# Performance work log

Hardware: AMD Instinct MI355X
Metric: run time of the kernel (lower is better)

Reference implementation:

```python
import jax, jax.numpy as jnp
import numpy as np
import math

EMBED_DIM = 64
NUM_HEADS = 4
HEAD_DIM = EMBED_DIM // NUM_HEADS
TGT = 64
SRC = 64
BSZ = 128


def setup_inputs() -> dict:
    key = jax.random.key(0)
    ks = jax.random.split(key, 8)
    x = jax.random.normal(ks[0], (TGT, BSZ, EMBED_DIM), dtype=jnp.float32)
    relation = jax.random.normal(ks[1], (TGT, SRC, BSZ, EMBED_DIM), dtype=jnp.float32)
    in_proj_weight = jax.random.normal(ks[2], (3 * EMBED_DIM, EMBED_DIM), dtype=jnp.float32) * 0.02
    in_proj_bias = jnp.zeros((3 * EMBED_DIM,), dtype=jnp.float32)
    rel_weight = jax.random.normal(ks[3], (2 * EMBED_DIM, EMBED_DIM), dtype=jnp.float32) * 0.02
    rel_bias = jnp.zeros((2 * EMBED_DIM,), dtype=jnp.float32)
    out_weight = jax.random.normal(ks[4], (EMBED_DIM, EMBED_DIM), dtype=jnp.float32) * 0.02
    out_bias = jnp.zeros((EMBED_DIM,), dtype=jnp.float32)
    return {
        'query': x, 'key': x, 'value': x, 'relation': relation,
        'in_proj_weight': in_proj_weight, 'in_proj_bias': in_proj_bias,
        'rel_weight': rel_weight, 'rel_bias': rel_bias,
        'out_weight': out_weight, 'out_bias': out_bias,
    }


def reference(query, key, value, relation, in_proj_weight, in_proj_bias,
              rel_weight, rel_bias, out_weight, out_bias):
    E, H, hd = EMBED_DIM, NUM_HEADS, HEAD_DIM
    t, b, _ = query.shape
    s = key.shape[0]
    scaling = hd ** (-0.5)
    # qkv projections (slices of the fused in_proj weight, as in _in_proj)
    q = query @ in_proj_weight[:E].T + in_proj_bias[:E]
    k = key @ in_proj_weight[E:2 * E].T + in_proj_bias[E:2 * E]
    v = value @ in_proj_weight[2 * E:].T + in_proj_bias[2 * E:]
    q = q.reshape(t, b * H, hd)
    k = k.reshape(s, b * H, hd)
    v = v.reshape(s, b * H, hd)
    # relation projection -> ra, rb, each [t, s, b*H, hd], then transpose(0,1)
    rel = relation @ rel_weight.T + rel_bias  # [t, s, b, 2E]
    ra = rel[..., :E].reshape(t, s, b * H, hd).swapaxes(0, 1)  # [s, t, bH, hd]
    rb = rel[..., E:].reshape(t, s, b * H, hd).swapaxes(0, 1)
    # q[i,j] = q[i] + ra_t[i,j]; requires t == s (broadcast as in torch)
    qp = (q[:, None] + ra) * scaling            # [t, s, bH, hd]
    kp = k[None, :] + rb                        # [t, s, bH, hd]
    attn_weights = jnp.einsum('ijbn,ijbn->ijb', qp, kp) * (1.0 / math.sqrt(hd))
    attn_weights = jax.nn.softmax(attn_weights, axis=1)
    attn = jnp.einsum('ijb,jbn->bin', attn_weights, v)  # [bH, t, hd]
    attn = attn.swapaxes(0, 1).reshape(t, b, E)
    out = attn @ out_weight.T + out_bias
    return out
```

## Files before the change

### kernel.cpp

```cpp
#include <hip/hip_runtime.h>
#include <hip/hip_bf16.h>

#define T_ 64
#define S_ 64
#define B_ 128
#define E_ 64
#define H_ 4

typedef float f32x4 __attribute__((ext_vector_type(4)));
typedef short bf16x8 __attribute__((ext_vector_type(8)));

static __device__ __forceinline__ short f2b(float f) {
    union { __hip_bfloat16 h; short s; } u;
    u.h = __float2bfloat16(f);
    return u.s;
}

__global__ __launch_bounds__(256) void k_qkv(
    const float* __restrict__ qin, const float* __restrict__ kin,
    const float* __restrict__ vin, const float* __restrict__ W,
    const float* __restrict__ bias, float* __restrict__ qkv)
{
    __shared__ float xs[3][32 * 68];
    __shared__ float WTs[64 * 68];
    const int tid = threadIdx.x;
    const int row0 = blockIdx.x * 32;

    #pragma unroll
    for (int l = 0; l < 6; ++l) {
        int f4 = l * 256 + tid;
        int src = f4 >> 9, rem = f4 & 511;
        int r = rem >> 4, e0 = (rem & 15) << 2;
        const float* xin = (src == 0) ? qin : (src == 1 ? kin : vin);
        float4 xv = reinterpret_cast<const float4*>(xin)[(size_t)(row0 + r) * 16 + (e0 >> 2)];
        float* dst = &xs[src][r * 68];
        dst[e0] = xv.x; dst[e0 + 1] = xv.y; dst[e0 + 2] = xv.z; dst[e0 + 3] = xv.w;
    }

    const int rq = tid >> 5, og = tid & 31;
    const int r0 = rq * 4, op0 = og * 2;

    for (int seg = 0; seg < 3; ++seg) {
        __syncthreads();
        #pragma unroll
        for (int l = 0; l < 4; ++l) {
            int f4 = l * 256 + tid;
            int o = f4 >> 4, e0 = (f4 & 15) << 2;
            float4 wv = reinterpret_cast<const float4*>(W)[(size_t)(seg * 64 + o) * 16 + (e0 >> 2)];
            WTs[(e0 + 0) * 68 + o] = wv.x; WTs[(e0 + 1) * 68 + o] = wv.y;
            WTs[(e0 + 2) * 68 + o] = wv.z; WTs[(e0 + 3) * 68 + o] = wv.w;
        }
        __syncthreads();

        float acc[4][2];
        #pragma unroll
        for (int rr = 0; rr < 4; ++rr) {
            acc[rr][0] = bias[seg * 64 + op0];
            acc[rr][1] = bias[seg * 64 + op0 + 1];
        }
        const float* xsrc = xs[seg];
        #pragma unroll 4
        for (int e = 0; e < 64; ++e) {
            float w0 = WTs[e * 68 + op0];
            float w1 = WTs[e * 68 + op0 + 1];
            #pragma unroll
            for (int rr = 0; rr < 4; ++rr) {
                float xv = xsrc[(r0 + rr) * 68 + e];
                acc[rr][0] += xv * w0;
                acc[rr][1] += xv * w1;
            }
        }
        #pragma unroll
        for (int rr = 0; rr < 4; ++rr) {
            float2 ov = make_float2(acc[rr][0], acc[rr][1]);
            reinterpret_cast<float2*>(
                &qkv[((size_t)seg * T_ * B_ + row0 + r0 + rr) * E_ + op0])[0] = ov;
        }
    }
}

__global__ __launch_bounds__(512, 2) void k_logits_mfma(
    const float* __restrict__ rel, const float* __restrict__ relW,
    const float* __restrict__ relBias, const float* __restrict__ qkv,
    float* __restrict__ logits)
{
    __shared__ char Bs[16384];

    const int tid = threadIdx.x;
    const int w   = tid >> 6;
    const int l   = tid & 63;
    const int c   = l & 15;
    const int rq  = l >> 4;
    const int i   = blockIdx.x >> 3;
    const int jb  = (blockIdx.x & 7) * 8;

    #pragma unroll
    for (int li = 0; li < 4; ++li) {
        int f4 = li * 512 + tid;
        int o = f4 >> 4, e4 = f4 & 15;
        float4 wv = reinterpret_cast<const float4*>(relW)[f4];
        ushort4 bv;
        bv.x = (ushort)f2b(wv.x); bv.y = (ushort)f2b(wv.y);
        bv.z = (ushort)f2b(wv.z); bv.w = (ushort)f2b(wv.w);
        int ot = o >> 4, cc = o & 15;
        int ks = e4 >> 3, rqb = (e4 & 7) >> 1, half = e4 & 1;
        int dest = (ot * 2 + ks) * 1024 + (rqb * 16 + cc) * 16 + half * 8;
        *reinterpret_cast<ushort4*>(Bs + dest) = bv;
    }

    float qpre[4][4], bbv[4];
    {
        const float* qrow = qkv + (size_t)i * (B_ * E_);
        #pragma unroll
        for (int h = 0; h < 4; ++h) {
            float ba = relBias[h * 16 + c];
            bbv[h] = relBias[64 + h * 16 + c];
            #pragma unroll
            for (int r = 0; r < 4; ++r) {
                int b = w * 16 + rq * 4 + r;
                qpre[h][r] = qrow[b * E_ + h * 16 + c] + ba;
            }
        }
    }
    __syncthreads();

    const int arow = ((w * 16 + c) * E_) + rq * 8;
    const int kbase = (w * 16 + rq * 4) * E_;

    float lbuf[8];
    float4 a0, a1, a2, a3;
    {
        const float* ab = rel + ((size_t)jb * S_ + i) * (size_t)(B_ * E_) + arow;
        a0 = *(const float4*)(ab);
        a1 = *(const float4*)(ab + 4);
        a2 = *(const float4*)(ab + 32);
        a3 = *(const float4*)(ab + 36);
    }

    #pragma unroll 1
    for (int t = 0; t < 8; ++t) {
        const int j = jb + t;

        bf16x8 af[2];
        {
            bf16x8 a;
            a[0] = f2b(a0.x); a[1] = f2b(a0.y); a[2] = f2b(a0.z); a[3] = f2b(a0.w);
            a[4] = f2b(a1.x); a[5] = f2b(a1.y); a[6] = f2b(a1.z); a[7] = f2b(a1.w);
            af[0] = a;
            a[0] = f2b(a2.x); a[1] = f2b(a2.y); a[2] = f2b(a2.z); a[3] = f2b(a2.w);
            a[4] = f2b(a3.x); a[5] = f2b(a3.y); a[6] = f2b(a3.z); a[7] = f2b(a3.w);
            af[1] = a;
        }

        if (t < 7) {
            const float* ab = rel + ((size_t)(j + 1) * S_ + i) * (size_t)(B_ * E_) + arow;
            a0 = *(const float4*)(ab);
            a1 = *(const float4*)(ab + 4);
            a2 = *(const float4*)(ab + 32);
            a3 = *(const float4*)(ab + 36);
        }

        float kvv[4][4];
        {
            const float* krow = qkv + ((size_t)(T_ * B_) + (size_t)j * B_) * E_ + kbase;
            #pragma unroll
            for (int h = 0; h < 4; ++h)
                #pragma unroll
                for (int r = 0; r < 4; ++r)
                    kvv[h][r] = krow[r * E_ + h * 16 + c];
        }

        f32x4 acc[8];
        #pragma unroll
        for (int ot = 0; ot < 8; ++ot) acc[ot] = (f32x4){0.f, 0.f, 0.f, 0.f};
        #pragma unroll
        for (int ot = 0; ot < 8; ++ot) {
            #pragma unroll
            for (int ks = 0; ks < 2; ++ks) {
                bf16x8 bfr = *(const bf16x8*)(Bs + (ot * 2 + ks) * 1024 + l * 16);
                acc[ot] = __builtin_amdgcn_mfma_f32_16x16x32_bf16(af[ks], bfr, acc[ot], 0, 0, 0);
            }
        }

        float v[16];
        #pragma unroll
        for (int h = 0; h < 4; ++h)
            #pragma unroll
            for (int r = 0; r < 4; ++r)
                v[h * 4 + r] = (qpre[h][r] + acc[h][r]) *
                               (kvv[h][r] + bbv[h] + acc[4 + h][r]);
        #pragma unroll
        for (int k = 0; k < 8; ++k) {
            float x = (c & 1) ? v[2 * k + 1] : v[2 * k];
            float y = (c & 1) ? v[2 * k] : v[2 * k + 1];
            v[k] = x + __shfl_xor(y, 1);
        }
        #pragma unroll
        for (int k = 0; k < 4; ++k) {
            float x = (c & 2) ? v[2 * k + 1] : v[2 * k];
            float y = (c & 2) ? v[2 * k] : v[2 * k + 1];
            v[k] = x + __shfl_xor(y, 2);
        }
        #pragma unroll
        for (int k = 0; k < 2; ++k) {
            float x = (c & 4) ? v[2 * k + 1] : v[2 * k];
            float y = (c & 4) ? v[2 * k] : v[2 * k + 1];
            v[k] = x + __shfl_xor(y, 4);
        }
        {
            float x = (c & 8) ? v[1] : v[0];
            float y = (c & 8) ? v[0] : v[1];
            lbuf[t] = (x + __shfl_xor(y, 8)) * 0.0625f;
        }
    }

    {
        const int hh = c >> 2, rr = c & 3;
        const int b = w * 16 + rq * 4 + rr;
        float* dst = &logits[(((size_t)i * B_ + b) * H_ + hh) * S_ + jb];
        *reinterpret_cast<float4*>(dst) = make_float4(lbuf[0], lbuf[1], lbuf[2], lbuf[3]);
        *reinterpret_cast<float4*>(dst + 4) = make_float4(lbuf[4], lbuf[5], lbuf[6], lbuf[7]);
    }
}

__global__ __launch_bounds__(256) void k_attn(
    const float* __restrict__ logits, const float* __restrict__ qkv,
    const float* __restrict__ Wout, const float* __restrict__ bout,
    float* __restrict__ out)
{
    __shared__ float wsm[4][H_][S_];
    __shared__ float ap[4][68];
    const int tid = threadIdx.x;
    const int i = blockIdx.x >> 5;
    const int bq = blockIdx.x & 31;
    const int w = tid >> 6, l = tid & 63;
    const int b = bq * 4 + w;

    const float* lg = logits + ((size_t)i * B_ + b) * H_ * S_;
    const int h = l >> 4, sub = l & 15;
    float v0 = lg[h * S_ + sub];
    float v1 = lg[h * S_ + sub + 16];
    float v2 = lg[h * S_ + sub + 32];
    float v3 = lg[h * S_ + sub + 48];
    float m = fmaxf(fmaxf(v0, v1), fmaxf(v2, v3));
    #pragma unroll
    for (int d = 1; d < 16; d <<= 1) m = fmaxf(m, __shfl_xor(m, d));
    float e0 = expf(v0 - m), e1 = expf(v1 - m), e2 = expf(v2 - m), e3 = expf(v3 - m);
    float ss = e0 + e1 + e2 + e3;
    #pragma unroll
    for (int d = 1; d < 16; d <<= 1) ss += __shfl_xor(ss, d);
    float inv = 1.0f / ss;
    wsm[w][h][sub] = e0 * inv;
    wsm[w][h][sub + 16] = e1 * inv;
    wsm[w][h][sub + 32] = e2 * inv;
    wsm[w][h][sub + 48] = e3 * inv;
    __syncthreads();

    const float* vbase = qkv + (size_t)2 * T_ * B_ * E_ + (size_t)b * E_;
    const float* wrow = &wsm[w][l >> 4][0];
    float acc = 0.f;
    #pragma unroll 4
    for (int j = 0; j < S_; ++j) acc += wrow[j] * vbase[(size_t)j * B_ * E_ + l];
    ap[w][l] = acc;
    __syncthreads();

    const float* wo = Wout + l * E_;
    const float* apw = ap[w];
    float oacc = bout[l];
    #pragma unroll 4
    for (int e = 0; e < E_; ++e) oacc += apw[e] * wo[e];
    out[((size_t)i * B_ + b) * E_ + l] = oacc;
}

extern "C" void kernel_launch(void* const* d_in, const int* in_sizes, int n_in,
                              void* d_out, int out_size, void* d_ws, size_t ws_size,
                              hipStream_t stream)
{
    const float* qin = (const float*)d_in[0];
    const float* kin = (const float*)d_in[1];
    const float* vin = (const float*)d_in[2];
    const float* rel = (const float*)d_in[3];
    const float* ipw = (const float*)d_in[4];
    const float* ipb = (const float*)d_in[5];
    const float* rw  = (const float*)d_in[6];
    const float* rb  = (const float*)d_in[7];
    const float* ow  = (const float*)d_in[8];
    const float* obias = (const float*)d_in[9];

    float* qkv = (float*)d_ws;
    float* logits = qkv + 3 * T_ * B_ * E_;
    float* out = (float*)d_out;

    k_qkv<<<dim3(256), dim3(256), 0, stream>>>(qin, kin, vin, ipw, ipb, qkv);
    k_logits_mfma<<<dim3(512), dim3(512), 0, stream>>>(rel, rw, rb, qkv, logits);
    k_attn<<<dim3(2048), dim3(256), 0, stream>>>(logits, qkv, ow, obias, out);
}
```

Measured before the change: 68.99 us.

## Double-buffer relation loads, hoist B fragments to registers in logits kernel

The logits kernel now prefetches relation rows two steps ahead using two register buffers and a manually 2x-unrolled loop. It hoists all B-operand weight fragments from LDS into registers once, instead of rereading them every iteration. Per-step logits go to an LDS scratch array rather than a register array. Launch bounds drop from two blocks per CU to one to make room for the extra registers, which lowers occupancy and latency hiding in exchange for deeper prefetch.

```diff
diff --git a/kernel.cpp b/kernel.cpp
--- a/kernel.cpp
+++ b/kernel.cpp
@@ -79,12 +79,13 @@
     }
 }
 
-__global__ __launch_bounds__(512, 2) void k_logits_mfma(
+__global__ __launch_bounds__(512, 1) void k_logits_mfma(
     const float* __restrict__ rel, const float* __restrict__ relW,
     const float* __restrict__ relBias, const float* __restrict__ qkv,
     float* __restrict__ logits)
 {
-    __shared__ char Bs[16384];
+    __shared__ char  Bs[16384];
+    __shared__ float llds[8][64][9];
 
     const int tid = threadIdx.x;
     const int w   = tid >> 6;
@@ -124,102 +125,109 @@
     }
     __syncthreads();
 
+    bf16x8 bfr[8][2];
+    #pragma unroll
+    for (int ot = 0; ot < 8; ++ot)
+        #pragma unroll
+        for (int ks = 0; ks < 2; ++ks)
+            bfr[ot][ks] = *(const bf16x8*)(Bs + (ot * 2 + ks) * 1024 + l * 16);
+
     const int arow = ((w * 16 + c) * E_) + rq * 8;
     const int kbase = (w * 16 + rq * 4) * E_;
 
-    float lbuf[8];
-    float4 a0, a1, a2, a3;
+#define LOADA(jj, X0, X1, X2, X3)                                              \
+    {                                                                          \
+        const float* ab = rel + ((size_t)(jj) * S_ + i) * (size_t)(B_ * E_) + arow; \
+        X0 = *(const float4*)(ab);                                             \
+        X1 = *(const float4*)(ab + 4);                                         \
+        X2 = *(const float4*)(ab + 32);                                        \
+        X3 = *(const float4*)(ab + 36);                                        \
+    }
+
+#define BODY(t, X0, X1, X2, X3)                                                \
+    {                                                                          \
+        const int j = jb + (t);                                                \
+        float kvv[4][4];                                                       \
+        {                                                                      \
+            const float* krow = qkv + ((size_t)(T_ * B_) + (size_t)j * B_) * E_ + kbase; \
+            _Pragma("unroll")                                                  \
+            for (int h = 0; h < 4; ++h)                                        \
+                _Pragma("unroll")                                              \
+                for (int r = 0; r < 4; ++r)                                    \
+                    kvv[h][r] = krow[r * E_ + h * 16 + c];                     \
+        }                                                                      \
+        bf16x8 af0, af1;                                                       \
+        {                                                                      \
+            bf16x8 a;                                                          \
+            a[0] = f2b(X0.x); a[1] = f2b(X0.y); a[2] = f2b(X0.z); a[3] = f2b(X0.w); \
+            a[4] = f2b(X1.x); a[5] = f2b(X1.y); a[6] = f2b(X1.z); a[7] = f2b(X1.w); \
+            af0 = a;                                                           \
+            a[0] = f2b(X2.x); a[1] = f2b(X2.y); a[2] = f2b(X2.z); a[3] = f2b(X2.w); \
+            a[4] = f2b(X3.x); a[5] = f2b(X3.y); a[6] = f2b(X3.z); a[7] = f2b(X3.w); \
+            af1 = a;                                                           \
+        }                                                                      \
+        if ((t) + 2 < 8) { LOADA(jb + (t) + 2, X0, X1, X2, X3) }               \
+        f32x4 acc[8];                                                          \
+        _Pragma("unroll")                                                      \
+        for (int ot = 0; ot < 8; ++ot) acc[ot] = (f32x4){0.f, 0.f, 0.f, 0.f};  \
+        _Pragma("unroll")                                                      \
+        for (int ot = 0; ot < 8; ++ot) {                                       \
+            acc[ot] = __builtin_amdgcn_mfma_f32_16x16x32_bf16(af0, bfr[ot][0], acc[ot], 0, 0, 0); \
+            acc[ot] = __builtin_amdgcn_mfma_f32_16x16x32_bf16(af1, bfr[ot][1], acc[ot], 0, 0, 0); \
+        }                                                                      \
+        float v[16];                                                           \
+        _Pragma("unroll")                                                      \
+        for (int h = 0; h < 4; ++h)                                            \
+            _Pragma("unroll")                                                  \
+            for (int r = 0; r < 4; ++r)                                        \
+                v[h * 4 + r] = (qpre[h][r] + acc[h][r]) *                      \
+                               (kvv[h][r] + bbv[h] + acc[4 + h][r]);           \
+        _Pragma("unroll")                                                      \
+        for (int k = 0; k < 8; ++k) {                                          \
+            float x = (c & 1) ? v[2 * k + 1] : v[2 * k];                       \
+            float y = (c & 1) ? v[2 * k] : v[2 * k + 1];                       \
+            v[k] = x + __shfl_xor(y, 1);                                       \
+        }                                                                      \
+        _Pragma("unroll")                                                      \
+        for (int k = 0; k < 4; ++k) {                                          \
+            float x = (c & 2) ? v[2 * k + 1] : v[2 * k];                       \
+            float y = (c & 2) ? v[2 * k] : v[2 * k + 1];                       \
+            v[k] = x + __shfl_xor(y, 2);                                       \
+        }                                                                      \
+        _Pragma("unroll")                                                      \
+        for (int k = 0; k < 2; ++k) {                                          \
+            float x = (c & 4) ? v[2 * k + 1] : v[2 * k];                       \
+            float y = (c & 4) ? v[2 * k] : v[2 * k + 1];                       \
+            v[k] = x + __shfl_xor(y, 4);                                       \
+        }                                                                      \
+        {                                                                      \
+            float x = (c & 8) ? v[1] : v[0];                                   \
+            float y = (c & 8) ? v[0] : v[1];                                   \
+            llds[w][l][(t)] = (x + __shfl_xor(y, 8)) * 0.0625f;                \
+        }                                                                      \
+    }
+
+    float4 aA0, aA1, aA2, aA3, aB0, aB1, aB2, aB3;
+    LOADA(jb + 0, aA0, aA1, aA2, aA3)
+    LOADA(jb + 1, aB0, aB1, aB2, aB3)
+
+    #pragma unroll 1
+    for (int tt = 0; tt < 8; tt += 2) {
+        BODY(tt,     aA0, aA1, aA2, aA3)
+        BODY(tt + 1, aB0, aB1, aB2, aB3)
+    }
+#undef BODY
+#undef LOADA
+
     {
-        const float* ab = rel + ((size_t)jb * S_ + i) * (size_t)(B_ * E_) + arow;
-        a0 = *(const float4*)(ab);
-        a1 = *(const float4*)(ab + 4);
-        a2 = *(const float4*)(ab + 32);
-        a3 = *(const float4*)(ab + 36);
-    }
-
-    #pragma unroll 1
-    for (int t = 0; t < 8; ++t) {
-        const int j = jb + t;
-
-        bf16x8 af[2];
-        {
-            bf16x8 a;
-            a[0] = f2b(a0.x); a[1] = f2b(a0.y); a[2] = f2b(a0.z); a[3] = f2b(a0.w);
-            a[4] = f2b(a1.x); a[5] = f2b(a1.y); a[6] = f2b(a1.z); a[7] = f2b(a1.w);
-            af[0] = a;
-            a[0] = f2b(a2.x); a[1] = f2b(a2.y); a[2] = f2b(a2.z); a[3] = f2b(a2.w);
-            a[4] = f2b(a3.x); a[5] = f2b(a3.y); a[6] = f2b(a3.z); a[7] = f2b(a3.w);
-            af[1] = a;
-        }
-
-        if (t < 7) {
-            const float* ab = rel + ((size_t)(j + 1) * S_ + i) * (size_t)(B_ * E_) + arow;
-            a0 = *(const float4*)(ab);
-            a1 = *(const float4*)(ab + 4);
-            a2 = *(const float4*)(ab + 32);
-            a3 = *(const float4*)(ab + 36);
-        }
-
-        float kvv[4][4];
-        {
-            const float* krow = qkv + ((size_t)(T_ * B_) + (size_t)j * B_) * E_ + kbase;
-            #pragma unroll
-            for (int h = 0; h < 4; ++h)
-                #pragma unroll
-                for (int r = 0; r < 4; ++r)
-                    kvv[h][r] = krow[r * E_ + h * 16 + c];
-        }
-
-        f32x4 acc[8];
-        #pragma unroll
-        for (int ot = 0; ot < 8; ++ot) acc[ot] = (f32x4){0.f, 0.f, 0.f, 0.f};
-        #pragma unroll
-        for (int ot = 0; ot < 8; ++ot) {
-            #pragma unroll
-            for (int ks = 0; ks < 2; ++ks) {
-                bf16x8 bfr = *(const bf16x8*)(Bs + (ot * 2 + ks) * 1024 + l * 16);
-                acc[ot] = __builtin_amdgcn_mfma_f32_16x16x32_bf16(af[ks], bfr, acc[ot], 0, 0, 0);
-            }
-        }
-
-        float v[16];
-        #pragma unroll
-        for (int h = 0; h < 4; ++h)
-            #pragma unroll
-            for (int r = 0; r < 4; ++r)
-                v[h * 4 + r] = (qpre[h][r] + acc[h][r]) *
-                               (kvv[h][r] + bbv[h] + acc[4 + h][r]);
-        #pragma unroll
-        for (int k = 0; k < 8; ++k) {
-            float x = (c & 1) ? v[2 * k + 1] : v[2 * k];
-            float y = (c & 1) ? v[2 * k] : v[2 * k + 1];
-            v[k] = x + __shfl_xor(y, 1);
-        }
-        #pragma unroll
-        for (int k = 0; k < 4; ++k) {
-            float x = (c & 2) ? v[2 * k + 1] : v[2 * k];
-            float y = (c & 2) ? v[2 * k] : v[2 * k + 1];
-            v[k] = x + __shfl_xor(y, 2);
-        }
-        #pragma unroll
-        for (int k = 0; k < 2; ++k) {
-            float x = (c & 4) ? v[2 * k + 1] : v[2 * k];
-            float y = (c & 4) ? v[2 * k] : v[2 * k + 1];
-            v[k] = x + __shfl_xor(y, 4);
-        }
-        {
-            float x = (c & 8) ? v[1] : v[0];
-            float y = (c & 8) ? v[0] : v[1];
-            lbuf[t] = (x + __shfl_xor(y, 8)) * 0.0625f;
-        }
-    }
-
-    {
+        float f[8];
+        #pragma unroll
+        for (int t2 = 0; t2 < 8; ++t2) f[t2] = llds[w][l][t2];
         const int hh = c >> 2, rr = c & 3;
         const int b = w * 16 + rq * 4 + rr;
         float* dst = &logits[(((size_t)i * B_ + b) * H_ + hh) * S_ + jb];
-        *reinterpret_cast<float4*>(dst) = make_float4(lbuf[0], lbuf[1], lbuf[2], lbuf[3]);
-        *reinterpret_cast<float4*>(dst + 4) = make_float4(lbuf[4], lbuf[5], lbuf[6], lbuf[7]);
+        *reinterpret_cast<float4*>(dst) = make_float4(f[0], f[1], f[2], f[3]);
+        *reinterpret_cast<float4*>(dst + 4) = make_float4(f[4], f[5], f[6], f[7]);
     }
 }
 
```

Result: no change. 70.24 us (+1.8%).

## Split logits kernel into one block per (i,j,half-batch) and relayout logits

Applied to the files above, without the earlier changes.

The logits kernel no longer loops over 8 source positions per block with software prefetch. Each 256-thread block now handles a single (i, j) pair and half the batch, launched as 8192 blocks. The logits buffer is laid out as [t][s][b*H] so each block writes one contiguous row, and the softmax kernel reads with a strided pattern to match. This buys more parallelism and latency hiding across blocks, at the cost of converting the rel weights to bf16 into shared memory once per block instead of once per 8 positions, and of uncoalesced logit reads in the attention kernel.

```diff
diff --git a/kernel.cpp b/kernel.cpp
--- a/kernel.cpp
+++ b/kernel.cpp
@@ -79,7 +79,7 @@
     }
 }
 
-__global__ __launch_bounds__(512, 2) void k_logits_mfma(
+__global__ __launch_bounds__(256, 3) void k_logits_mfma(
     const float* __restrict__ rel, const float* __restrict__ relW,
     const float* __restrict__ relBias, const float* __restrict__ qkv,
     float* __restrict__ logits)
@@ -91,12 +91,24 @@
     const int l   = tid & 63;
     const int c   = l & 15;
     const int rq  = l >> 4;
-    const int i   = blockIdx.x >> 3;
-    const int jb  = (blockIdx.x & 7) * 8;
-
-    #pragma unroll
-    for (int li = 0; li < 4; ++li) {
-        int f4 = li * 512 + tid;
+    const int g   = blockIdx.x & 1;
+    const int j   = (blockIdx.x >> 1) & 63;
+    const int i   = blockIdx.x >> 7;
+    const int btile = g * 4 + w;
+
+    const int arow = ((btile * 16 + c) * E_) + rq * 8;
+    float4 a0, a1, a2, a3;
+    {
+        const float* ab = rel + ((size_t)j * S_ + i) * (size_t)(B_ * E_) + arow;
+        a0 = *(const float4*)(ab);
+        a1 = *(const float4*)(ab + 4);
+        a2 = *(const float4*)(ab + 32);
+        a3 = *(const float4*)(ab + 36);
+    }
+
+    #pragma unroll
+    for (int li = 0; li < 8; ++li) {
+        int f4 = li * 256 + tid;
         int o = f4 >> 4, e4 = f4 & 15;
         float4 wv = reinterpret_cast<const float4*>(relW)[f4];
         ushort4 bv;
@@ -117,109 +129,80 @@
             bbv[h] = relBias[64 + h * 16 + c];
             #pragma unroll
             for (int r = 0; r < 4; ++r) {
-                int b = w * 16 + rq * 4 + r;
+                int b = btile * 16 + rq * 4 + r;
                 qpre[h][r] = qrow[b * E_ + h * 16 + c] + ba;
             }
         }
     }
     __syncthreads();
 
-    const int arow = ((w * 16 + c) * E_) + rq * 8;
-    const int kbase = (w * 16 + rq * 4) * E_;
-
-    float lbuf[8];
-    float4 a0, a1, a2, a3;
-    {
-        const float* ab = rel + ((size_t)jb * S_ + i) * (size_t)(B_ * E_) + arow;
-        a0 = *(const float4*)(ab);
-        a1 = *(const float4*)(ab + 4);
-        a2 = *(const float4*)(ab + 32);
-        a3 = *(const float4*)(ab + 36);
-    }
-
-    #pragma unroll 1
-    for (int t = 0; t < 8; ++t) {
-        const int j = jb + t;
-
-        bf16x8 af[2];
-        {
-            bf16x8 a;
-            a[0] = f2b(a0.x); a[1] = f2b(a0.y); a[2] = f2b(a0.z); a[3] = f2b(a0.w);
-            a[4] = f2b(a1.x); a[5] = f2b(a1.y); a[6] = f2b(a1.z); a[7] = f2b(a1.w);
-            af[0] = a;
-            a[0] = f2b(a2.x); a[1] = f2b(a2.y); a[2] = f2b(a2.z); a[3] = f2b(a2.w);
-            a[4] = f2b(a3.x); a[5] = f2b(a3.y); a[6] = f2b(a3.z); a[7] = f2b(a3.w);
-            af[1] = a;
-        }
-
-        if (t < 7) {
-            const float* ab = rel + ((size_t)(j + 1) * S_ + i) * (size_t)(B_ * E_) + arow;
-            a0 = *(const float4*)(ab);
-            a1 = *(const float4*)(ab + 4);
-            a2 = *(const float4*)(ab + 32);
-            a3 = *(const float4*)(ab + 36);
-        }
-
-        float kvv[4][4];
-        {
-            const float* krow = qkv + ((size_t)(T_ * B_) + (size_t)j * B_) * E_ + kbase;
-            #pragma unroll
-            for (int h = 0; h < 4; ++h)
-                #pragma unroll
-                for (int r = 0; r < 4; ++r)
-                    kvv[h][r] = krow[r * E_ + h * 16 + c];
-        }
-
-        f32x4 acc[8];
-        #pragma unroll
-        for (int ot = 0; ot < 8; ++ot) acc[ot] = (f32x4){0.f, 0.f, 0.f, 0.f};
-        #pragma unroll
-        for (int ot = 0; ot < 8; ++ot) {
-            #pragma unroll
-            for (int ks = 0; ks < 2; ++ks) {
-                bf16x8 bfr = *(const bf16x8*)(Bs + (ot * 2 + ks) * 1024 + l * 16);
-                acc[ot] = __builtin_amdgcn_mfma_f32_16x16x32_bf16(af[ks], bfr, acc[ot], 0, 0, 0);
-            }
-        }
-
-        float v[16];
+    float kvv[4][4];
+    {
+        const float* krow = qkv + ((size_t)(T_ * B_) + (size_t)j * B_ + btile * 16 + rq * 4) * E_;
         #pragma unroll
         for (int h = 0; h < 4; ++h)
             #pragma unroll
             for (int r = 0; r < 4; ++r)
-                v[h * 4 + r] = (qpre[h][r] + acc[h][r]) *
-                               (kvv[h][r] + bbv[h] + acc[4 + h][r]);
-        #pragma unroll
-        for (int k = 0; k < 8; ++k) {
-            float x = (c & 1) ? v[2 * k + 1] : v[2 * k];
-            float y = (c & 1) ? v[2 * k] : v[2 * k + 1];
-            v[k] = x + __shfl_xor(y, 1);
-        }
-        #pragma unroll
-        for (int k = 0; k < 4; ++k) {
-            float x = (c & 2) ? v[2 * k + 1] : v[2 * k];
-            float y = (c & 2) ? v[2 * k] : v[2 * k + 1];
-            v[k] = x + __shfl_xor(y, 2);
-        }
-        #pragma unroll
-        for (int k = 0; k < 2; ++k) {
-            float x = (c & 4) ? v[2 * k + 1] : v[2 * k];
-            float y = (c & 4) ? v[2 * k] : v[2 * k + 1];
-            v[k] = x + __shfl_xor(y, 4);
-        }
-        {
-            float x = (c & 8) ? v[1] : v[0];
-            float y = (c & 8) ? v[0] : v[1];
-            lbuf[t] = (x + __shfl_xor(y, 8)) * 0.0625f;
-        }
-    }
-
-    {
-        const int hh = c >> 2, rr = c & 3;
-        const int b = w * 16 + rq * 4 + rr;
-        float* dst = &logits[(((size_t)i * B_ + b) * H_ + hh) * S_ + jb];
-        *reinterpret_cast<float4*>(dst) = make_float4(lbuf[0], lbuf[1], lbuf[2], lbuf[3]);
-        *reinterpret_cast<float4*>(dst + 4) = make_float4(lbuf[4], lbuf[5], lbuf[6], lbuf[7]);
+                kvv[h][r] = krow[r * E_ + h * 16 + c];
+    }
+
+    bf16x8 af0, af1;
+    {
+        bf16x8 a;
+        a[0] = f2b(a0.x); a[1] = f2b(a0.y); a[2] = f2b(a0.z); a[3] = f2b(a0.w);
+        a[4] = f2b(a1.x); a[5] = f2b(a1.y); a[6] = f2b(a1.z); a[7] = f2b(a1.w);
+        af0 = a;
+        a[0] = f2b(a2.x); a[1] = f2b(a2.y); a[2] = f2b(a2.z); a[3] = f2b(a2.w);
+        a[4] = f2b(a3.x); a[5] = f2b(a3.y); a[6] = f2b(a3.z); a[7] = f2b(a3.w);
+        af1 = a;
+    }
+
+    f32x4 acc[8];
+    #pragma unroll
+    for (int ot = 0; ot < 8; ++ot) acc[ot] = (f32x4){0.f, 0.f, 0.f, 0.f};
+    #pragma unroll
+    for (int ot = 0; ot < 8; ++ot) {
+        bf16x8 b0 = *(const bf16x8*)(Bs + (ot * 2 + 0) * 1024 + l * 16);
+        bf16x8 b1 = *(const bf16x8*)(Bs + (ot * 2 + 1) * 1024 + l * 16);
+        acc[ot] = __builtin_amdgcn_mfma_f32_16x16x32_bf16(af0, b0, acc[ot], 0, 0, 0);
+        acc[ot] = __builtin_amdgcn_mfma_f32_16x16x32_bf16(af1, b1, acc[ot], 0, 0, 0);
+    }
+
+    float v[16];
+    #pragma unroll
+    for (int h = 0; h < 4; ++h)
+        #pragma unroll
+        for (int r = 0; r < 4; ++r)
+            v[h * 4 + r] = (qpre[h][r] + acc[h][r]) *
+                           (kvv[h][r] + bbv[h] + acc[4 + h][r]);
+    #pragma unroll
+    for (int k = 0; k < 8; ++k) {
+        float x = (c & 1) ? v[2 * k + 1] : v[2 * k];
+        float y = (c & 1) ? v[2 * k] : v[2 * k + 1];
+        v[k] = x + __shfl_xor(y, 1);
+    }
+    #pragma unroll
+    for (int k = 0; k < 4; ++k) {
+        float x = (c & 2) ? v[2 * k + 1] : v[2 * k];
+        float y = (c & 2) ? v[2 * k] : v[2 * k + 1];
+        v[k] = x + __shfl_xor(y, 2);
+    }
+    #pragma unroll
+    for (int k = 0; k < 2; ++k) {
+        float x = (c & 4) ? v[2 * k + 1] : v[2 * k];
+        float y = (c & 4) ? v[2 * k] : v[2 * k + 1];
+        v[k] = x + __shfl_xor(y, 4);
+    }
+    float outv;
+    {
+        float x = (c & 8) ? v[1] : v[0];
+        float y = (c & 8) ? v[0] : v[1];
+        outv = (x + __shfl_xor(y, 8)) * 0.0625f;
+    }
+
+    {
+        const int off = btile * 64 + rq * 16 + (c & 3) * 4 + (c >> 2);
+        logits[((size_t)i * S_ + j) * (B_ * H_) + off] = outv;
     }
 }
 
@@ -236,12 +219,12 @@
     const int w = tid >> 6, l = tid & 63;
     const int b = bq * 4 + w;
 
-    const float* lg = logits + ((size_t)i * B_ + b) * H_ * S_;
     const int h = l >> 4, sub = l & 15;
-    float v0 = lg[h * S_ + sub];
-    float v1 = lg[h * S_ + sub + 16];
-    float v2 = lg[h * S_ + sub + 32];
-    float v3 = lg[h * S_ + sub + 48];
+    const float* lg = logits + (size_t)i * S_ * (B_ * H_) + b * H_ + h;
+    float v0 = lg[(size_t)(sub +  0) * (B_ * H_)];
+    float v1 = lg[(size_t)(sub + 16) * (B_ * H_)];
+    float v2 = lg[(size_t)(sub + 32) * (B_ * H_)];
+    float v3 = lg[(size_t)(sub + 48) * (B_ * H_)];
     float m = fmaxf(fmaxf(v0, v1), fmaxf(v2, v3));
     #pragma unroll
     for (int d = 1; d < 16; d <<= 1) m = fmaxf(m, __shfl_xor(m, d));
@@ -292,6 +275,6 @@
     float* out = (float*)d_out;
 
     k_qkv<<<dim3(256), dim3(256), 0, stream>>>(qin, kin, vin, ipw, ipb, qkv);
-    k_logits_mfma<<<dim3(512), dim3(512), 0, stream>>>(rel, rw, rb, qkv, logits);
+    k_logits_mfma<<<dim3(8192), dim3(256), 0, stream>>>(rel, rw, rb, qkv, logits);
     k_attn<<<dim3(2048), dim3(256), 0, stream>>>(logits, qkv, ow, obias, out);
 }
```

Measured after the change: 78.36 us. +13.6%, slower.

## Precompute bf16 rel weights and fold key+bias into MFMA via identity matrix

Applied to the files above, without the earlier changes.

An extra block in the QKV kernel converts the relation weight to bf16 in MFMA fragment layout once and builds an identity block. The K projection plus relation bias is written as packed bf16 fragments. The logits kernel then copies the weights straight into LDS and adds k+bias with an extra MFMA against the identity matrix, instead of scattered fp32 K loads and per-block weight conversion. Logit results are staged through LDS instead of registers. This lowers register pressure and global gather traffic, at the cost of extra MFMAs and bf16 rounding of k+bias.

```diff
diff --git a/kernel.cpp b/kernel.cpp
--- a/kernel.cpp
+++ b/kernel.cpp
@@ -19,11 +19,39 @@
 __global__ __launch_bounds__(256) void k_qkv(
     const float* __restrict__ qin, const float* __restrict__ kin,
     const float* __restrict__ vin, const float* __restrict__ W,
-    const float* __restrict__ bias, float* __restrict__ qkv)
+    const float* __restrict__ bias, float* __restrict__ qkv,
+    const float* __restrict__ relW, const float* __restrict__ relBias,
+    ushort* __restrict__ wBf, unsigned int* __restrict__ kpbW)
 {
+    const int tid = threadIdx.x;
+
+    if (blockIdx.x == 256) {
+        #pragma unroll
+        for (int li = 0; li < 8; ++li) {
+            int f4 = li * 256 + tid;
+            int o = f4 >> 4, e4 = f4 & 15;
+            float4 wv = reinterpret_cast<const float4*>(relW)[f4];
+            ushort4 bv;
+            bv.x = (ushort)f2b(wv.x); bv.y = (ushort)f2b(wv.y);
+            bv.z = (ushort)f2b(wv.z); bv.w = (ushort)f2b(wv.w);
+            int ot = o >> 4, cc = o & 15;
+            int ks = e4 >> 3, rqb = (e4 & 7) >> 1, half = e4 & 1;
+            int dest = (ot * 2 + ks) * 512 + (rqb * 16 + cc) * 8 + half * 4;
+            *reinterpret_cast<ushort4*>(wBf + dest) = bv;
+        }
+        #pragma unroll
+        for (int li = 0; li < 8; ++li) {
+            int t = li * 256 + tid;
+            int ot = t >> 9, lane = (t >> 3) & 63, e = t & 7;
+            int cI = lane & 15, rqI = lane >> 4;
+            wBf[8192 + t] =
+                (rqI * 8 + e == (ot & 1) * 16 + cI) ? (ushort)0x3F80 : (ushort)0;
+        }
+        return;
+    }
+
     __shared__ float xs[3][32 * 68];
     __shared__ float WTs[64 * 68];
-    const int tid = threadIdx.x;
     const int row0 = blockIdx.x * 32;
 
     #pragma unroll
@@ -76,110 +104,119 @@
             reinterpret_cast<float2*>(
                 &qkv[((size_t)seg * T_ * B_ + row0 + r0 + rr) * E_ + op0])[0] = ov;
         }
+        if (seg == 1) {
+            #pragma unroll
+            for (int rr = 0; rr < 4; ++rr) {
+                int row = row0 + r0 + rr;
+                int jj = row >> 7, b = row & 127;
+                float kb0 = acc[rr][0] + relBias[64 + op0];
+                float kb1 = acc[rr][1] + relBias[64 + op0 + 1];
+                unsigned int u = (unsigned int)(ushort)f2b(kb0) |
+                                 ((unsigned int)(ushort)f2b(kb1) << 16);
+                int off = jj * 8192 + (op0 >> 5) * 4096 + (b >> 4) * 512 +
+                          ((b & 15) + ((op0 & 31) >> 3) * 16) * 8 + (op0 & 7);
+                kpbW[off >> 1] = u;
+            }
+        }
     }
 }
 
 __global__ __launch_bounds__(512, 2) void k_logits_mfma(
-    const float* __restrict__ rel, const float* __restrict__ relW,
-    const float* __restrict__ relBias, const float* __restrict__ qkv,
-    float* __restrict__ logits)
+    const float* __restrict__ rel, const ushort* __restrict__ wBf,
+    const ushort* __restrict__ kpbF, const float* __restrict__ relBias,
+    const float* __restrict__ qkv, float* __restrict__ logits)
 {
-    __shared__ char Bs[16384];
+    __shared__ char  Bs[20480];
+    __shared__ float llds[8][64][9];
 
     const int tid = threadIdx.x;
-    const int w   = tid >> 6;
-    const int l   = tid & 63;
-    const int c   = l & 15;
-    const int rq  = l >> 4;
-    const int i   = blockIdx.x >> 3;
-    const int jb  = (blockIdx.x & 7) * 8;
+    const int w = tid >> 6, l = tid & 63;
+    const int c = l & 15, rq = l >> 4;
+    const int i = blockIdx.x >> 3;
+    const int jb = (blockIdx.x & 7) * 8;
 
     #pragma unroll
-    for (int li = 0; li < 4; ++li) {
-        int f4 = li * 512 + tid;
-        int o = f4 >> 4, e4 = f4 & 15;
-        float4 wv = reinterpret_cast<const float4*>(relW)[f4];
-        ushort4 bv;
-        bv.x = (ushort)f2b(wv.x); bv.y = (ushort)f2b(wv.y);
-        bv.z = (ushort)f2b(wv.z); bv.w = (ushort)f2b(wv.w);
-        int ot = o >> 4, cc = o & 15;
-        int ks = e4 >> 3, rqb = (e4 & 7) >> 1, half = e4 & 1;
-        int dest = (ot * 2 + ks) * 1024 + (rqb * 16 + cc) * 16 + half * 8;
-        *reinterpret_cast<ushort4*>(Bs + dest) = bv;
-    }
-
-    float qpre[4][4], bbv[4];
+    for (int li = 0; li < 3; ++li) {
+        int idx = li * 512 + tid;
+        if (idx < 1280)
+            reinterpret_cast<float4*>(Bs)[idx] =
+                reinterpret_cast<const float4*>(wBf)[idx];
+    }
+
+    float qpre[4][4];
     {
         const float* qrow = qkv + (size_t)i * (B_ * E_);
         #pragma unroll
         for (int h = 0; h < 4; ++h) {
             float ba = relBias[h * 16 + c];
-            bbv[h] = relBias[64 + h * 16 + c];
             #pragma unroll
-            for (int r = 0; r < 4; ++r) {
-                int b = w * 16 + rq * 4 + r;
-                qpre[h][r] = qrow[b * E_ + h * 16 + c] + ba;
-            }
+            for (int r = 0; r < 4; ++r)
+                qpre[h][r] = qrow[(w * 16 + rq * 4 + r) * E_ + h * 16 + c] + ba;
         }
     }
     __syncthreads();
 
-    const int arow = ((w * 16 + c) * E_) + rq * 8;
-    const int kbase = (w * 16 + rq * 4) * E_;
-
-    float lbuf[8];
-    float4 a0, a1, a2, a3;
+    const int arow = (w * 16 + c) * E_ + rq * 8;
+    const int kfo  = w * 512 + l * 8;
+
+    float4 x0, x1, x2, x3;
     {
         const float* ab = rel + ((size_t)jb * S_ + i) * (size_t)(B_ * E_) + arow;
-        a0 = *(const float4*)(ab);
-        a1 = *(const float4*)(ab + 4);
-        a2 = *(const float4*)(ab + 32);
-        a3 = *(const float4*)(ab + 36);
+        x0 = *(const float4*)(ab);
+        x1 = *(const float4*)(ab + 4);
+        x2 = *(const float4*)(ab + 32);
+        x3 = *(const float4*)(ab + 36);
     }
 
     #pragma unroll 1
     for (int t = 0; t < 8; ++t) {
         const int j = jb + t;
 
-        bf16x8 af[2];
+        bf16x8 kf0 = *(const bf16x8*)(kpbF + (size_t)j * 8192 + kfo);
+        bf16x8 kf1 = *(const bf16x8*)(kpbF + (size_t)j * 8192 + 4096 + kfo);
+
+        bf16x8 af0, af1;
         {
             bf16x8 a;
-            a[0] = f2b(a0.x); a[1] = f2b(a0.y); a[2] = f2b(a0.z); a[3] = f2b(a0.w);
-            a[4] = f2b(a1.x); a[5] = f2b(a1.y); a[6] = f2b(a1.z); a[7] = f2b(a1.w);
-            af[0] = a;
-            a[0] = f2b(a2.x); a[1] = f2b(a2.y); a[2] = f2b(a2.z); a[3] = f2b(a2.w);
-            a[4] = f2b(a3.x); a[5] = f2b(a3.y); a[6] = f2b(a3.z); a[7] = f2b(a3.w);
-            af[1] = a;
+            a[0] = f2b(x0.x); a[1] = f2b(x0.y); a[2] = f2b(x0.z); a[3] = f2b(x0.w);
+            a[4] = f2b(x1.x); a[5] = f2b(x1.y); a[6] = f2b(x1.z); a[7] = f2b(x1.w);
+            af0 = a;
+            a[0] = f2b(x2.x); a[1] = f2b(x2.y); a[2] = f2b(x2.z); a[3] = f2b(x2.w);
+            a[4] = f2b(x3.x); a[5] = f2b(x3.y); a[6] = f2b(x3.z); a[7] = f2b(x3.w);
+            af1 = a;
         }
 
         if (t < 7) {
             const float* ab = rel + ((size_t)(j + 1) * S_ + i) * (size_t)(B_ * E_) + arow;
-            a0 = *(const float4*)(ab);
-            a1 = *(const float4*)(ab + 4);
-            a2 = *(const float4*)(ab + 32);
-            a3 = *(const float4*)(ab + 36);
-        }
-
-        float kvv[4][4];
-        {
-            const float* krow = qkv + ((size_t)(T_ * B_) + (size_t)j * B_) * E_ + kbase;
-            #pragma unroll
-            for (int h = 0; h < 4; ++h)
-                #pragma unroll
-                for (int r = 0; r < 4; ++r)
-                    kvv[h][r] = krow[r * E_ + h * 16 + c];
-        }
+            x0 = *(const float4*)(ab);
+            x1 = *(const float4*)(ab + 4);
+            x2 = *(const float4*)(ab + 32);
+            x3 = *(const float4*)(ab + 36);
+        }
+
+        int bs0 = 0;
+        asm volatile("" : "+v"(bs0));
+        const char* bsp = Bs + bs0;
 
         f32x4 acc[8];
         #pragma unroll
         for (int ot = 0; ot < 8; ++ot) acc[ot] = (f32x4){0.f, 0.f, 0.f, 0.f};
         #pragma unroll
-        for (int ot = 0; ot < 8; ++ot) {
-            #pragma unroll
-            for (int ks = 0; ks < 2; ++ks) {
-                bf16x8 bfr = *(const bf16x8*)(Bs + (ot * 2 + ks) * 1024 + l * 16);
-                acc[ot] = __builtin_amdgcn_mfma_f32_16x16x32_bf16(af[ks], bfr, acc[ot], 0, 0, 0);
-            }
+        for (int ot = 0; ot < 4; ++ot) {
+            acc[ot] = __builtin_amdgcn_mfma_f32_16x16x32_bf16(
+                af0, *(const bf16x8*)(bsp + (ot * 2 + 0) * 1024 + l * 16), acc[ot], 0, 0, 0);
+            acc[ot] = __builtin_amdgcn_mfma_f32_16x16x32_bf16(
+                af1, *(const bf16x8*)(bsp + (ot * 2 + 1) * 1024 + l * 16), acc[ot], 0, 0, 0);
+        }
+        #pragma unroll
+        for (int ot = 0; ot < 4; ++ot) {
+            acc[4 + ot] = __builtin_amdgcn_mfma_f32_16x16x32_bf16(
+                af0, *(const bf16x8*)(bsp + (8 + ot * 2 + 0) * 1024 + l * 16), acc[4 + ot], 0, 0, 0);
+            acc[4 + ot] = __builtin_amdgcn_mfma_f32_16x16x32_bf16(
+                af1, *(const bf16x8*)(bsp + (8 + ot * 2 + 1) * 1024 + l * 16), acc[4 + ot], 0, 0, 0);
+            acc[4 + ot] = __builtin_amdgcn_mfma_f32_16x16x32_bf16(
+                (ot < 2 ? kf0 : kf1),
+                *(const bf16x8*)(bsp + (16 + ot) * 1024 + l * 16), acc[4 + ot], 0, 0, 0);
         }
 
         float v[16];
@@ -187,8 +224,7 @@
         for (int h = 0; h < 4; ++h)
             #pragma unroll
             for (int r = 0; r < 4; ++r)
-                v[h * 4 + r] = (qpre[h][r] + acc[h][r]) *
-                               (kvv[h][r] + bbv[h] + acc[4 + h][r]);
+                v[h * 4 + r] = (qpre[h][r] + acc[h][r]) * acc[4 + h][r];
         #pragma unroll
         for (int k = 0; k < 8; ++k) {
             float x = (c & 1) ? v[2 * k + 1] : v[2 * k];
@@ -210,16 +246,19 @@
         {
             float x = (c & 8) ? v[1] : v[0];
             float y = (c & 8) ? v[0] : v[1];
-            lbuf[t] = (x + __shfl_xor(y, 8)) * 0.0625f;
+            llds[w][l][t] = (x + __shfl_xor(y, 8)) * 0.0625f;
         }
     }
 
     {
+        float f[8];
+        #pragma unroll
+        for (int t2 = 0; t2 < 8; ++t2) f[t2] = llds[w][l][t2];
         const int hh = c >> 2, rr = c & 3;
         const int b = w * 16 + rq * 4 + rr;
         float* dst = &logits[(((size_t)i * B_ + b) * H_ + hh) * S_ + jb];
-        *reinterpret_cast<float4*>(dst) = make_float4(lbuf[0], lbuf[1], lbuf[2], lbuf[3]);
-        *reinterpret_cast<float4*>(dst + 4) = make_float4(lbuf[4], lbuf[5], lbuf[6], lbuf[7]);
+        *reinterpret_cast<float4*>(dst) = make_float4(f[0], f[1], f[2], f[3]);
+        *reinterpret_cast<float4*>(dst + 4) = make_float4(f[4], f[5], f[6], f[7]);
     }
 }
 
@@ -289,9 +328,13 @@
 
     float* qkv = (float*)d_ws;
     float* logits = qkv + 3 * T_ * B_ * E_;
+    ushort* wBf  = (ushort*)(logits + (size_t)T_ * S_ * B_ * H_);
+    ushort* kpbF = wBf + 16384;
+
     float* out = (float*)d_out;
 
-    k_qkv<<<dim3(256), dim3(256), 0, stream>>>(qin, kin, vin, ipw, ipb, qkv);
-    k_logits_mfma<<<dim3(512), dim3(512), 0, stream>>>(rel, rw, rb, qkv, logits);
+    k_qkv<<<dim3(257), dim3(256), 0, stream>>>(qin, kin, vin, ipw, ipb, qkv,
+                                               rw, rb, wBf, (unsigned int*)kpbF);
+    k_logits_mfma<<<dim3(512), dim3(512), 0, stream>>>(rel, wBf, kpbF, rb, qkv, logits);
     k_attn<<<dim3(2048), dim3(256), 0, stream>>>(logits, qkv, ow, obias, out);
 }
```

After: 66.08 us. 1.04x faster.
